# Kernel tuning notes

Measured on AMD Instinct MI355X. Metric: run time of the kernel, lower is better.

## Reference

```python
import jax, jax.numpy as jnp
import numpy as np

N_QUBITS = 4
N_LAYERS = 3
N_FEATURES = 64
BATCH = 524288


def setup_inputs() -> dict:
    key = jax.random.key(0)
    k1, k2, k3, k4 = jax.random.split(key, 4)
    x = jax.random.normal(k1, (BATCH, N_FEATURES), jnp.float32)
    # nn.Linear(64, 4) params
    lim = 1.0 / np.sqrt(N_FEATURES)
    W_pre = jax.random.uniform(k2, (N_QUBITS, N_FEATURES), jnp.float32, -lim, lim)
    b_pre = jax.random.uniform(k3, (N_QUBITS,), jnp.float32, -lim, lim)
    # quantum circuit weights: randn * 0.1
    qweights = jax.random.normal(k4, (N_LAYERS, N_QUBITS, 2), jnp.float32) * 0.1
    return {"x": x, "W_pre": W_pre, "b_pre": b_pre, "qweights": qweights}


def _coef(theta, n):
    # reshape scalar or [B] angle to broadcast against [B, 2,..,2] (n-1 trailing dims after slicing)
    return jnp.reshape(theta, (-1,) + (1,) * (n - 1))


def _apply_ry(state, wire, theta):
    # RY(t) = [[cos t/2, -sin t/2], [sin t/2, cos t/2]] applied on `wire`
    n = state.ndim - 1
    s = jnp.moveaxis(state, 1 + wire, -1)
    a, b = s[..., 0], s[..., 1]
    c = _coef(jnp.cos(theta / 2), n)
    sn = _coef(jnp.sin(theta / 2), n)
    out = jnp.stack([c * a - sn * b, sn * a + c * b], axis=-1)
    return jnp.moveaxis(out, -1, 1 + wire)


def _apply_rz(state, wire, theta):
    # RZ(t) = diag(e^{-i t/2}, e^{+i t/2})
    n = state.ndim - 1
    s = jnp.moveaxis(state, 1 + wire, -1)
    half = _coef(theta / 2, n)
    out = jnp.stack([jnp.exp(-1j * half) * s[..., 0],
                     jnp.exp(1j * half) * s[..., 1]], axis=-1)
    return jnp.moveaxis(out, -1, 1 + wire)


def _apply_cnot(state, ctrl, tgt):
    s = jnp.moveaxis(state, (1 + ctrl, 1 + tgt), (-2, -1))
    s = jnp.concatenate([s[..., 0:1, :], s[..., 1:2, ::-1]], axis=-2)
    return jnp.moveaxis(s, (-2, -1), (1 + ctrl, 1 + tgt))


def _circuit(angles, qweights):
    # batched 4-qubit statevector simulation; state shape [B, 2,2,2,2] (wire 0 = MSB)
    B, n = angles.shape
    nl = qweights.shape[0]
    state = jnp.zeros((B,) + (2,) * n, jnp.complex64)
    state = state.at[(slice(None),) + (0,) * n].set(1.0)
    for w in range(n):
        state = _apply_ry(state, w, angles[:, w])
    for l in range(nl):
        for w in range(n):
            state = _apply_ry(state, w, qweights[l, w, 0])
            state = _apply_rz(state, w, qweights[l, w, 1])
        for w in range(n):
            state = _apply_cnot(state, w, (w + 1) % n)
    probs = state.real ** 2 + state.imag ** 2  # [B, 2,2,2,2] float32
    exps = []
    for w in range(n):
        marg = jnp.moveaxis(probs, 1 + w, 1).reshape(B, 2, -1).sum(-1)  # [B, 2]
        exps.append(marg[:, 0] - marg[:, 1])  # <Z_w>
    return jnp.stack(exps, axis=1)  # [B, n]


def reference(x, W_pre, b_pre, qweights):
    angles = jnp.tanh(x @ W_pre.T + b_pre)  # [B, n_qubits]
    return _circuit(angles, qweights).astype(jnp.float32)
```

## Files before the change

### kernel.cpp

```cpp
#include <hip/hip_runtime.h>
#include <hip/hip_bf16.h>
#include <cmath>


typedef __attribute__((ext_vector_type(8))) short bf16x8;
typedef __attribute__((ext_vector_type(4))) float f32x4;

__global__ __launch_bounds__(256) void qprep_kernel(
    const float* __restrict__ qw,
    float* __restrict__ A_out)
{
  __shared__ float sre[16][17];
  __shared__ float sim[16][17];
  __shared__ float M[4][16][16];
  const int tid = threadIdx.x;
  const int col = tid >> 4;
  const int u   = tid & 15;

  sre[col][u] = (u == col) ? 1.0f : 0.0f;
  sim[col][u] = 0.0f;
  __syncthreads();

#pragma unroll
  for (int l = 0; l < 3; ++l) {
#pragma unroll
    for (int w = 0; w < 4; ++w) {
      const int mask = 8 >> w;
      float sh, ch, sh2, ch2;
      __sincosf(0.5f * qw[(l * 4 + w) * 2 + 0], &sh, &ch);
      __sincosf(0.5f * qw[(l * 4 + w) * 2 + 1], &sh2, &ch2);
      const int ua = u & ~mask, ub = u | mask;
      const float ar = sre[col][ua], ai = sim[col][ua];
      const float br = sre[col][ub], bi = sim[col][ub];
      __syncthreads();
      float nr, ni;
      if (u & mask) { nr = sh * ar + ch * br; ni = sh * ai + ch * bi; }
      else          { nr = ch * ar - sh * br; ni = ch * ai - sh * bi; }
      float rr, ri;
      if (u & mask) { rr = ch2 * nr - sh2 * ni; ri = ch2 * ni + sh2 * nr; }
      else          { rr = ch2 * nr + sh2 * ni; ri = ch2 * ni - sh2 * nr; }
      sre[col][u] = rr; sim[col][u] = ri;
      __syncthreads();
    }
    int src = u;
    if (src & 1) src ^= 8;
    if (src & 2) src ^= 1;
    if (src & 4) src ^= 2;
    if (src & 8) src ^= 4;
    const float pr = sre[col][src], pi = sim[col][src];
    __syncthreads();
    sre[col][u] = pr; sim[col][u] = pi;
    __syncthreads();
  }

  for (int idx = tid; idx < 1024; idx += 256) {
    const int w = idx >> 8, s = (idx >> 4) & 15, t = idx & 15;
    const int mask = 8 >> w;
    float acc = 0.0f;
#pragma unroll
    for (int uu = 0; uu < 16; ++uu) {
      const float z = (uu & mask) ? -1.0f : 1.0f;
      acc += z * (sre[s][uu] * sre[t][uu] + sim[s][uu] * sim[t][uu]);
    }
    M[w][s][t] = acc;
  }
  __syncthreads();

  for (int idx = tid; idx < 324; idx += 256) {
    const int w = idx & 3, pq = idx >> 2;
    const int p = pq / 9, q = pq % 9;
    const int i0 = p / 3, i1 = p % 3, i2 = q / 3, i3 = q % 3;
    float acc = 0.0f;
#pragma unroll
    for (int comb = 0; comb < 16; ++comb) {
      int s = 0, t = 0;
      float coef = 0.0625f;
      int j;
      j = (comb >> 3) & 1; s |= j << 3; t |= ((i0 == 2) ? (j ^ 1) : j) << 3; if (i0 == 1 && j) coef = -coef;
      j = (comb >> 2) & 1; s |= j << 2; t |= ((i1 == 2) ? (j ^ 1) : j) << 2; if (i1 == 1 && j) coef = -coef;
      j = (comb >> 1) & 1; s |= j << 1; t |= ((i2 == 2) ? (j ^ 1) : j) << 1; if (i2 == 1 && j) coef = -coef;
      j = comb & 1;        s |= j;      t |= ((i3 == 2) ? (j ^ 1) : j);      if (i3 == 1 && j) coef = -coef;
      acc = fmaf(coef, M[w][s][t], acc);
    }
    A_out[idx] = acc;
  }
}

__device__ __forceinline__ bf16x8 pack8(const float4 va, const float4 vb) {
  union { bf16x8 v; __hip_bfloat16 h[8]; } u;
  u.h[0] = __float2bfloat16(va.x); u.h[1] = __float2bfloat16(va.y);
  u.h[2] = __float2bfloat16(va.z); u.h[3] = __float2bfloat16(va.w);
  u.h[4] = __float2bfloat16(vb.x); u.h[5] = __float2bfloat16(vb.y);
  u.h[6] = __float2bfloat16(vb.z); u.h[7] = __float2bfloat16(vb.w);
  return u.v;
}

__device__ __forceinline__ float ftanh(float a) {
  return 1.0f - 2.0f * __builtin_amdgcn_rcpf(__expf(2.0f * a) + 1.0f);
}

#define ISSUE(S, R0, R1, R2, R3) {                                          \
  const float4* g_ = xs4 + (wrow0 + (size_t)((S) * 16)) * 16 + lane;        \
  R0 = g_[0]; R1 = g_[64]; R2 = g_[128]; R3 = g_[192]; }

#define WRITE(R0, R1, R2, R3, S) {                                          \
  float* d_ = sb + ((S) & 1) * 1024;                                        \
  *reinterpret_cast<float4*>(d_ + wsA)        = R0;                         \
  *reinterpret_cast<float4*>(d_ + wsB + 256)  = R1;                         \
  *reinterpret_cast<float4*>(d_ + wsA + 512)  = R2;                         \
  *reinterpret_cast<float4*>(d_ + wsB + 768)  = R3; }

#define CONSUME(S) {                                                        \
  const float* s_ = sb + ((S) & 1) * 1024;                                  \
  const float4 f0 = *reinterpret_cast<const float4*>(s_ + ((cb_ + 0) ^ rw_)); \
  const float4 f1 = *reinterpret_cast<const float4*>(s_ + ((cb_ + 4) ^ rw_)); \
  const float4 f2 = *reinterpret_cast<const float4*>(s_ + ((cb_ + 32) ^ rw_)); \
  const float4 f3 = *reinterpret_cast<const float4*>(s_ + ((cb_ + 36) ^ rw_)); \
  const bf16x8 af0_ = pack8(f0, f1);                                        \
  const bf16x8 af1_ = pack8(f2, f3);                                        \
  f32x4 acc_ = __builtin_amdgcn_mfma_f32_16x16x32_bf16(af0_, wf0, zero, 0, 0, 0); \
  acc_ = __builtin_amdgcn_mfma_f32_16x16x32_bf16(af1_, wf1, acc_, 0, 0, 0); \
  if (arow < 4) {                                                           \
    _Pragma("unroll")                                                       \
    for (int r_ = 0; r_ < 4; ++r_)                                          \
      ap[((((S) & 3) * 16) + kgrp * 4 + r_) * 4 + arow] = acc_[r_];         \
  } }

#define TAIL(R0) {                                                          \
  asm volatile("s_waitcnt lgkmcnt(0)" ::: "memory");                        \
  __builtin_amdgcn_sched_barrier(0);                                        \
  const float4 ang = *reinterpret_cast<const float4*>(&ap[lane * 4]);       \
  const float t0 = ftanh(ang.x + bp[0]);                                    \
  const float t1 = ftanh(ang.y + bp[1]);                                    \
  const float t2 = ftanh(ang.z + bp[2]);                                    \
  const float t3 = ftanh(ang.w + bp[3]);                                    \
  float c0, s0, c1, s1, c2, s2, c3, s3;                                     \
  __sincosf(t0, &s0, &c0); __sincosf(t1, &s1, &c1);                         \
  __sincosf(t2, &s2, &c2); __sincosf(t3, &s3, &c3);                         \
  const float g[9] = {1.f, c1, s1, c0, c0 * c1, c0 * s1,                    \
                      s0, s0 * c1, s0 * s1};                                \
  const float h[9] = {1.f, c3, s3, c2, c2 * c3, c2 * s3,                    \
                      s2, s2 * c3, s2 * s3};                                \
  float e0 = 0.f, e1 = 0.f, e2 = 0.f, e3 = 0.f;                             \
  _Pragma("unroll")                                                         \
  for (int p_ = 0; p_ < 9; ++p_) {                                          \
    _Pragma("unroll")                                                       \
    for (int q_ = 0; q_ < 9; ++q_) {                                        \
      const float4 a4 = Aws[p_ * 9 + q_];                                   \
      const float tt = g[p_] * h[q_];                                       \
      e0 = fmaf(a4.x, tt, e0); e1 = fmaf(a4.y, tt, e1);                     \
      e2 = fmaf(a4.z, tt, e2); e3 = fmaf(a4.w, tt, e3);                     \
    }                                                                       \
  }                                                                         \
  reinterpret_cast<float4*>(out)[(R0) + lane] =                             \
      make_float4(e0, e1, e2, e3);                                          \
  asm volatile("" ::: "memory"); }

__global__ __launch_bounds__(256)
__attribute__((amdgpu_waves_per_eu(4, 4)))
void qmain_kernel(
    const float* __restrict__ x,
    const float* __restrict__ Wp,
    const float* __restrict__ bp,
    const float4* __restrict__ Aws,
    float* __restrict__ out)
{
  __shared__ alignas(16) float lds[4 * 2304];

  const int tid  = threadIdx.x;
  const int lane = tid & 63;
  const int wid  = tid >> 6;
  const int arow = lane & 15;
  const int kgrp = lane >> 4;
  float* sb = &lds[wid * 2304];
  float* ap = sb + 2048;

  const size_t wrow0 = ((size_t)blockIdx.x * 4 + wid) * 128;
  const float4* xs4 = reinterpret_cast<const float4*>(x);

  const int wsA = (lane * 4) ^ ((lane >> 4) << 2);
  const int wsB = (lane * 4) ^ (((lane >> 4) + 4) << 2);
  const int rw_ = (arow & 7) << 2;
  const int cb_ = arow * 64 + kgrp * 8;

  bf16x8 wf0, wf1;
#pragma unroll
  for (int j = 0; j < 8; ++j) {
    if (arow < 4) {
      union { short s; __hip_bfloat16 h; } u0, u1;
      u0.h = __float2bfloat16(Wp[arow * 64 + 0  + kgrp * 8 + j]);
      u1.h = __float2bfloat16(Wp[arow * 64 + 32 + kgrp * 8 + j]);
      wf0[j] = u0.s; wf1[j] = u1.s;
    } else {
      wf0[j] = 0; wf1[j] = 0;
    }
  }
  const f32x4 zero = {0.f, 0.f, 0.f, 0.f};

  const size_t r0 = wrow0;
  const size_t r1 = wrow0 + 64;

  float4 A0, A1, A2, A3, B0, B1, B2, B3, C0, C1, C2, C3;

  ISSUE(0, A0, A1, A2, A3);
  ISSUE(1, B0, B1, B2, B3);
  ISSUE(2, C0, C1, C2, C3);
  WRITE(A0, A1, A2, A3, 0);
  WRITE(B0, B1, B2, B3, 1);
  CONSUME(0); ISSUE(3, A0, A1, A2, A3); WRITE(C0, C1, C2, C3, 2);
  CONSUME(1); ISSUE(4, B0, B1, B2, B3); WRITE(A0, A1, A2, A3, 3);
  CONSUME(2); ISSUE(5, C0, C1, C2, C3); WRITE(B0, B1, B2, B3, 4);
  CONSUME(3); ISSUE(6, A0, A1, A2, A3); WRITE(C0, C1, C2, C3, 5);

  TAIL(r0);

  CONSUME(4); ISSUE(7, B0, B1, B2, B3); WRITE(A0, A1, A2, A3, 6);
  CONSUME(5); WRITE(B0, B1, B2, B3, 7);
  CONSUME(6);
  CONSUME(7);

  TAIL(r1);
}

extern "C" void kernel_launch(void* const* d_in, const int* in_sizes, int n_in,
                              void* d_out, int out_size, void* d_ws, size_t ws_size,
                              hipStream_t stream) {
  const float* x  = (const float*)d_in[0];
  const float* Wp = (const float*)d_in[1];
  const float* bp = (const float*)d_in[2];
  const float* qw = (const float*)d_in[3];
  float* out = (float*)d_out;
  float* A = (float*)d_ws;
  (void)n_in; (void)out_size; (void)ws_size;

  qprep_kernel<<<1, 256, 0, stream>>>(qw, A);

  const int B = in_sizes[0] / 64;
  qmain_kernel<<<B / 512, 256, 0, stream>>>(x, Wp, bp,
                                            (const float4*)A, out);
}
```

Baseline: 34.96 us.

## Stream x tiles directly into LDS with global_load_lds and waitcnt pipeline

Replaces the register-staged global loads and LDS writes with direct global-to-LDS loads. The XOR swizzle moves to the global source address, and manual vmcnt/lgkmcnt waits drive a double-buffered schedule. This is meant to save the VGPRs and LDS write instructions spent staging x through registers. In exchange the pipeline holds only two stages in flight instead of three, and correctness now depends on hand-written waitcnt values, including around the TAIL's own memory ops.

Measured after the change: 35.82 us. 2.5% more time.

```diff
diff --git a/kernel.cpp b/kernel.cpp
--- a/kernel.cpp
+++ b/kernel.cpp
@@ -99,16 +99,24 @@
   return 1.0f - 2.0f * __builtin_amdgcn_rcpf(__expf(2.0f * a) + 1.0f);
 }
 
-#define ISSUE(S, R0, R1, R2, R3) {                                          \
-  const float4* g_ = xs4 + (wrow0 + (size_t)((S) * 16)) * 16 + lane;        \
-  R0 = g_[0]; R1 = g_[64]; R2 = g_[128]; R3 = g_[192]; }
-
-#define WRITE(R0, R1, R2, R3, S) {                                          \
-  float* d_ = sb + ((S) & 1) * 1024;                                        \
-  *reinterpret_cast<float4*>(d_ + wsA)        = R0;                         \
-  *reinterpret_cast<float4*>(d_ + wsB + 256)  = R1;                         \
-  *reinterpret_cast<float4*>(d_ + wsA + 512)  = R2;                         \
-  *reinterpret_cast<float4*>(d_ + wsB + 768)  = R3; }
+__device__ __forceinline__ void gll16(const float* g, float* l) {
+  __builtin_amdgcn_global_load_lds(
+      (const __attribute__((address_space(1))) void*)g,
+      (__attribute__((address_space(3))) void*)l, 16, 0, 0);
+}
+
+#define STAGE(S) {                                                          \
+  const float* gb_ = x + (wrow0 + (size_t)((S) * 16)) * 64;                 \
+  float* lb_ = sb + ((S) & 1) * 1024;                                       \
+  gll16(gb_ + (((0 * 256 + lane * 4) ^ ((((0 * 4) + (lane >> 4)) & 7) << 2))), lb_ + 0 * 256); \
+  gll16(gb_ + (((1 * 256 + lane * 4) ^ ((((1 * 4) + (lane >> 4)) & 7) << 2))), lb_ + 1 * 256); \
+  gll16(gb_ + (((2 * 256 + lane * 4) ^ ((((2 * 4) + (lane >> 4)) & 7) << 2))), lb_ + 2 * 256); \
+  gll16(gb_ + (((3 * 256 + lane * 4) ^ ((((3 * 4) + (lane >> 4)) & 7) << 2))), lb_ + 3 * 256); }
+
+#define VM(N) { asm volatile("s_waitcnt vmcnt(" #N ")" ::: "memory");       \
+                __builtin_amdgcn_sched_barrier(0); }
+#define LG0() { asm volatile("s_waitcnt lgkmcnt(0)" ::: "memory");          \
+                __builtin_amdgcn_sched_barrier(0); }
 
 #define CONSUME(S) {                                                        \
   const float* s_ = sb + ((S) & 1) * 1024;                                  \
@@ -176,10 +184,6 @@
   float* ap = sb + 2048;
 
   const size_t wrow0 = ((size_t)blockIdx.x * 4 + wid) * 128;
-  const float4* xs4 = reinterpret_cast<const float4*>(x);
-
-  const int wsA = (lane * 4) ^ ((lane >> 4) << 2);
-  const int wsB = (lane * 4) ^ (((lane >> 4) + 4) << 2);
   const int rw_ = (arow & 7) << 2;
   const int cb_ = arow * 64 + kgrp * 8;
 
@@ -200,24 +204,25 @@
   const size_t r0 = wrow0;
   const size_t r1 = wrow0 + 64;
 
-  float4 A0, A1, A2, A3, B0, B1, B2, B3, C0, C1, C2, C3;
-
-  ISSUE(0, A0, A1, A2, A3);
-  ISSUE(1, B0, B1, B2, B3);
-  ISSUE(2, C0, C1, C2, C3);
-  WRITE(A0, A1, A2, A3, 0);
-  WRITE(B0, B1, B2, B3, 1);
-  CONSUME(0); ISSUE(3, A0, A1, A2, A3); WRITE(C0, C1, C2, C3, 2);
-  CONSUME(1); ISSUE(4, B0, B1, B2, B3); WRITE(A0, A1, A2, A3, 3);
-  CONSUME(2); ISSUE(5, C0, C1, C2, C3); WRITE(B0, B1, B2, B3, 4);
-  CONSUME(3); ISSUE(6, A0, A1, A2, A3); WRITE(C0, C1, C2, C3, 5);
+  STAGE(0);
+  STAGE(1);
+  VM(4);  CONSUME(0);
+  LG0();  STAGE(2);
+  VM(4);  CONSUME(1);
+  LG0();  STAGE(3);
+  VM(4);  CONSUME(2);
+  LG0();  STAGE(4);
+  VM(4);  CONSUME(3);
+  LG0();  STAGE(5);
 
   TAIL(r0);
 
-  CONSUME(4); ISSUE(7, B0, B1, B2, B3); WRITE(A0, A1, A2, A3, 6);
-  CONSUME(5); WRITE(B0, B1, B2, B3, 7);
-  CONSUME(6);
-  CONSUME(7);
+  VM(5);  CONSUME(4);
+  LG0();  STAGE(6);
+  VM(5);  CONSUME(5);
+  LG0();  STAGE(7);
+  VM(4);  CONSUME(6);
+  VM(0);  CONSUME(7);
 
   TAIL(r1);
 }
```
